# Kernel tuning notes

Hardware: AMD Instinct MI355X
Metric: run time of the kernel (lower is better)

Reference implementation:

```python
import jax, jax.numpy as jnp
import numpy as np
import math

HASHMAP_SIZE = 1 << 17
N_LEVELS = 16
N_FEATURES = 2
BASE_RES = 16.0
GROWTH = 1.5  # per-level resolution growth factor
PRIME_Y = np.uint32(2654435761)  # Instant-NGP spatial hash prime


def hash_encode(x, encoding):
    """Multiresolution 2D hash-grid encoding with bilinear interpolation.
    x: [N, 2] in [0,1); encoding: [T, L, F]. Returns [N, L*F]."""
    N = x.shape[0]
    scales = jnp.asarray(BASE_RES * GROWTH ** np.arange(N_LEVELS),
                         dtype=x.dtype)  # [L]
    pos = x[:, None, :] * scales[None, :, None]        # [N, L, 2]
    pf = jnp.floor(pos)
    frac = pos - pf                                    # [N, L, 2]
    pi = pf.astype(jnp.uint32)                         # integer corner base
    lvl = jnp.arange(N_LEVELS)[None, :]                # [1, L]

    feat = jnp.zeros((N, N_LEVELS, N_FEATURES), dtype=x.dtype)
    for cx in (0, 1):
        for cy in (0, 1):
            ix = pi[..., 0] + jnp.uint32(cx)
            iy = pi[..., 1] + jnp.uint32(cy)
            h = ix ^ (iy * PRIME_Y)                    # spatial hash (wraps mod 2^32)
            idx = (h & jnp.uint32(HASHMAP_SIZE - 1)).astype(jnp.int32)  # [N, L]
            wx = frac[..., 0] if cx else 1.0 - frac[..., 0]
            wy = frac[..., 1] if cy else 1.0 - frac[..., 1]
            feat = feat + (wx * wy)[..., None] * encoding[idx, lvl]  # gather [N,L,F]
    return feat.reshape(N, N_LEVELS * N_FEATURES)


def setup_inputs() -> dict:
    key = jax.random.key(0)
    ks = jax.random.split(key, 8)
    N = 1 << 20
    n_neurons = [32, 64, 64, 3]
    x = jax.random.uniform(ks[0], (N, 2), dtype=jnp.float32)
    # encoding init: rand * 2e-4 - 1e-4
    encoding = jax.random.uniform(ks[1], (HASHMAP_SIZE, N_LEVELS, N_FEATURES),
                                  dtype=jnp.float32) * 2e-4 - 1e-4
    inp = {"x": x, "encoding": encoding}
    for i in range(3):
        s = 1.0 / math.sqrt(n_neurons[i])
        w = jax.random.uniform(ks[2 + i], (n_neurons[i], n_neurons[i + 1]),
                               dtype=jnp.float32) * 2 * s - s
        b = jax.random.uniform(ks[5 + i], (n_neurons[i + 1],),
                               dtype=jnp.float32) * 2 * s - s
        inp[f"w{i}"] = w
        inp[f"b{i}"] = b
    return inp


def reference(x, encoding, w0, b0, w1, b1, w2, b2):
    feat = hash_encode(x, encoding)                 # [N, 32]
    h = jax.nn.relu(feat @ w0 + b0)                 # [N, 64]
    h = jax.nn.relu(h @ w1 + b1)                    # [N, 64]
    return h @ w2 + b2                              # [N, 3]
```

## Files before the change

### kernel.cpp

```cpp
#include <hip/hip_runtime.h>
#include <stdint.h>

typedef __bf16 bf16_t;
typedef bf16_t bf16x8 __attribute__((ext_vector_type(8)));
typedef float  f32x4  __attribute__((ext_vector_type(4)));
typedef float  f32x2v __attribute__((ext_vector_type(2)));

static constexpr uint32_t PRIME = 2654435761u;
static constexpr uint32_t HMASK = (1u << 17) - 1u;
static constexpr uint32_t TSIZE = 1u << 17;

static constexpr int NLDS   = 5308;
static constexpr int NDALL  = 136642;

static constexpr float FSCALE = 8192.0f;
static constexpr float WSCALE = 1.0f / 8192.0f;

__device__ __forceinline__ uint32_t fbits(float f) {
    union { float f; uint32_t u; } v; v.f = f; return v.u;
}
__device__ __forceinline__ float asfloat(uint32_t u) {
    union { uint32_t u; float f; } v; v.u = u; return v.f;
}

__device__ __forceinline__ uint32_t enc8(float v) {
    const uint32_t s = (fbits(v) >> 24) & 0x80u;
    float m = fabsf(v) * 0x1p-120f;
    uint32_t u = fbits(m);
    u += 0x7FFFFu + ((u >> 20) & 1u);
    return s | ((u >> 20) & 0x7fu);
}
__device__ __forceinline__ uint32_t pack8(float a, float b) {
#if __has_builtin(__builtin_amdgcn_cvt_pk_fp8_f32)
    return (uint32_t)__builtin_amdgcn_cvt_pk_fp8_f32(a, b, 0, false) & 0xffffu;
#else
    return enc8(a) | (enc8(b) << 8);
#endif
}
__device__ __forceinline__ float2 unpack8(uint32_t u) {
#if __has_builtin(__builtin_amdgcn_cvt_pk_f32_fp8)
    f32x2v r = __builtin_amdgcn_cvt_pk_f32_fp8((int)u, false);
    return make_float2(r.x, r.y);
#else
    const float f0 = asfloat(((u & 0x80u) << 24) | ((u & 0x7fu) << 20)) * 0x1p120f;
    const float f1 = asfloat(((u & 0x8000u) << 16) | ((u & 0x7f00u) << 12)) * 0x1p120f;
    return make_float2(f0, f1);
#endif
}

__global__ __launch_bounds__(256)
void repack_enc8(const float2* __restrict__ src, uint16_t* __restrict__ dst) {
    __shared__ uint16_t ldsT[8 * 257];
    const int tid = threadIdx.x;
    const int t0  = blockIdx.x * 256;
#pragma unroll
    for (int k = 0; k < 8; ++k) {
        const int j = k * 256 + tid;
        const int tl = j >> 3, l8 = j & 7;
        const float2 f = src[((size_t)(t0 + tl) << 4) + 8 + l8];
        ldsT[l8 * 257 + tl] = (uint16_t)pack8(f.x * FSCALE, f.y * FSCALE);
    }
    __syncthreads();
#pragma unroll
    for (int k = 0; k < 8; ++k)
        dst[((uint32_t)k << 17) + t0 + tid] = ldsT[k * 257 + tid];
}

__global__ __launch_bounds__(256)
void densify_enc(const float2* __restrict__ src, uint16_t* __restrict__ dst) {
    const int i = blockIdx.x * 256 + threadIdx.x;
    if (i >= NDALL) return;
    int lvl, W, off;
    if      (i <   289) { lvl = 0; W =  17; off = 0;     }
    else if (i <   914) { lvl = 1; W =  25; off = 289;   }
    else if (i <  2283) { lvl = 2; W =  37; off = 914;   }
    else if (i <  5308) { lvl = 3; W =  55; off = 2283;  }
    else if (i < 12032) { lvl = 4; W =  82; off = 5308;  }
    else if (i < 27161) { lvl = 5; W = 123; off = 12032; }
    else if (i < 61017) { lvl = 6; W = 184; off = 27161; }
    else                { lvl = 7; W = 275; off = 61017; }
    const int li = i - off;
    const uint32_t iy = (uint32_t)(li / W), ix = (uint32_t)(li % W);
    const uint32_t h = (ix ^ (iy * PRIME)) & HMASK;
    const float2 f = src[h * 16 + lvl];
    dst[i] = (uint16_t)pack8(f.x * FSCALE, f.y * FSCALE);
}

__global__ __launch_bounds__(256)
void pairify_enc(const uint16_t* __restrict__ d16, uint32_t* __restrict__ dst) {
    const int i = blockIdx.x * 256 + threadIdx.x;
    if (i >= NDALL) return;
    const uint32_t a = d16[i];
    const uint32_t b = (i + 1 < NDALL) ? d16[i + 1] : 0u;
    dst[i] = a | (b << 16);
}

__global__ __launch_bounds__(256, 2)
void fused_hash_mlp(const float* __restrict__ xin,
                    const uint16_t* __restrict__ tab8,
                    const uint32_t* __restrict__ dpair,
                    const float* __restrict__ w0, const float* __restrict__ b0,
                    const float* __restrict__ w1, const float* __restrict__ b1,
                    const float* __restrict__ w2, const float* __restrict__ b2,
                    float* __restrict__ out,
                    int nGroups)
{
    __shared__ uint32_t ldsTab[NLDS];
    __shared__ __align__(16) bf16_t lds[4 * 16 * 80];

    const int tid  = threadIdx.x;
    const int wib  = tid >> 6;
    const int lane = tid & 63;
    const int q    = lane >> 4;
    const int n16  = lane & 15;

    bf16_t* myLds = &lds[wib * (16 * 80)];

    for (int i = tid; i < NLDS; i += 256) ldsTab[i] = dpair[i];

    bf16x8 Bw0[4], Bw1[2][4], Bw2[2];
#pragma unroll
    for (int t = 0; t < 4; ++t)
#pragma unroll
        for (int j = 0; j < 8; ++j)
            Bw0[t][j] = (bf16_t)(w0[(q * 8 + j) * 64 + t * 16 + n16] * WSCALE);
#pragma unroll
    for (int c = 0; c < 2; ++c)
#pragma unroll
        for (int t = 0; t < 4; ++t)
#pragma unroll
            for (int j = 0; j < 8; ++j)
                Bw1[c][t][j] = (bf16_t)w1[(c * 32 + q * 8 + j) * 64 + t * 16 + n16];
#pragma unroll
    for (int c = 0; c < 2; ++c)
#pragma unroll
        for (int j = 0; j < 8; ++j)
            Bw2[c][j] = (n16 < 3) ? (bf16_t)w2[(c * 32 + q * 8 + j) * 3 + n16]
                                  : (bf16_t)0.0f;

    float bv0[4], bv1[4];
#pragma unroll
    for (int t = 0; t < 4; ++t) {
        bv0[t] = b0[t * 16 + n16];
        bv1[t] = b1[t * 16 + n16];
    }
    const float bv2 = (n16 < 3) ? b2[n16] : 0.0f;

    const float sb = 16.0f * ((q == 0) ? 1.0f :
                              (q == 1) ? 5.0625f :
                              (q == 2) ? 25.62890625f :
                                         129.746337890625f);
    const float sc[4] = { sb, sb * 1.5f, sb * 2.25f, sb * 3.375f };

    const uint32_t l8base = ((uint32_t)((q >= 2 ? q - 2 : 0) * 4)) << 17;

    __syncthreads();

    for (int g = blockIdx.x; g < nGroups; g += gridDim.x) {
        const int tile = g * 4 + wib;
        const int p = tile * 16 + n16;
        const float2 xy = ((const float2*)xin)[p];
        const float px = xy.x, py = xy.y;

        bf16x8 af;
#pragma unroll
        for (int lv = 0; lv < 4; ++lv) {
            const float posx = px * sc[lv], posy = py * sc[lv];
            const float fx = floorf(posx), fy = floorf(posy);
            const float frx = posx - fx,  fry = posy - fy;
            const uint32_t ix = (uint32_t)fx, iy = (uint32_t)fy;

            const uint32_t Wl = (lv == 0) ? 17u  : (lv == 1) ? 25u
                              : (lv == 2) ? 37u  : 55u;
            const uint32_t Ol = (lv == 0) ? 0u   : (lv == 1) ? 289u
                              : (lv == 2) ? 914u : 2283u;
            const uint32_t Wg = (lv == 0) ? 82u    : (lv == 1) ? 123u
                              : (lv == 2) ? 184u   : 275u;
            const uint32_t Og = (lv == 0) ? 5308u  : (lv == 1) ? 12032u
                              : (lv == 2) ? 27161u : 61017u;

            uint32_t u00, u10, u01, u11;
            if (q == 0) {
                const uint32_t a  = Ol + iy * Wl + ix;
                const uint32_t p0 = ldsTab[a];
                const uint32_t p1 = ldsTab[a + Wl];
                u00 = p0 & 0xffffu; u10 = p0 >> 16;
                u01 = p1 & 0xffffu; u11 = p1 >> 16;
            } else if (q == 1) {
                const uint32_t a  = Og + iy * Wg + ix;
                const uint32_t p0 = dpair[a];
                const uint32_t p1 = dpair[a + Wg];
                u00 = p0 & 0xffffu; u10 = p0 >> 16;
                u01 = p1 & 0xffffu; u11 = p1 >> 16;
            } else {
                const uint32_t hy0 = iy * PRIME, hy1 = hy0 + PRIME;
                const uint32_t i00 = ( ix       ^ hy0) & HMASK;
                const uint32_t i10 = ((ix + 1u) ^ hy0) & HMASK;
                const uint32_t i01 = ( ix       ^ hy1) & HMASK;
                const uint32_t i11 = ((ix + 1u) ^ hy1) & HMASK;
                const uint32_t base = l8base + ((uint32_t)lv << 17);
                u00 = tab8[base + i00];
                u10 = tab8[base + i10];
                u01 = tab8[base + i01];
                u11 = tab8[base + i11];
            }

            const float2 e00 = unpack8(u00);
            const float2 e10 = unpack8(u10);
            const float2 e01 = unpack8(u01);
            const float2 e11 = unpack8(u11);
            const float wx1 = frx, wx0 = 1.0f - frx, wy1 = fry, wy0 = 1.0f - fry;
            const float w00 = wx0 * wy0, w10 = wx1 * wy0, w01 = wx0 * wy1, w11 = wx1 * wy1;
            const float f0 = w00 * e00.x + w10 * e10.x + w01 * e01.x + w11 * e11.x;
            const float f1 = w00 * e00.y + w10 * e10.y + w01 * e01.y + w11 * e11.y;
            af[2 * lv]     = (bf16_t)f0;
            af[2 * lv + 1] = (bf16_t)f1;
        }

        f32x4 c0[4];
#pragma unroll
        for (int t = 0; t < 4; ++t) {
            f32x4 cc = { bv0[t], bv0[t], bv0[t], bv0[t] };
            c0[t] = __builtin_amdgcn_mfma_f32_16x16x32_bf16(af, Bw0[t], cc, 0, 0, 0);
        }

#pragma unroll
        for (int t = 0; t < 4; ++t)
#pragma unroll
            for (int r = 0; r < 4; ++r)
                myLds[(q * 4 + r) * 80 + t * 16 + n16] = (bf16_t)fmaxf(c0[t][r], 0.0f);

        bf16x8 A1[2];
#pragma unroll
        for (int c = 0; c < 2; ++c)
            A1[c] = *(const bf16x8*)&myLds[n16 * 80 + c * 32 + q * 8];

        f32x4 c1[4];
#pragma unroll
        for (int t = 0; t < 4; ++t) {
            f32x4 cc = { bv1[t], bv1[t], bv1[t], bv1[t] };
            cc    = __builtin_amdgcn_mfma_f32_16x16x32_bf16(A1[0], Bw1[0][t], cc, 0, 0, 0);
            c1[t] = __builtin_amdgcn_mfma_f32_16x16x32_bf16(A1[1], Bw1[1][t], cc, 0, 0, 0);
        }

#pragma unroll
        for (int t = 0; t < 4; ++t)
#pragma unroll
            for (int r = 0; r < 4; ++r)
                myLds[(q * 4 + r) * 80 + t * 16 + n16] = (bf16_t)fmaxf(c1[t][r], 0.0f);

        bf16x8 A2[2];
#pragma unroll
        for (int c = 0; c < 2; ++c)
            A2[c] = *(const bf16x8*)&myLds[n16 * 80 + c * 32 + q * 8];

        f32x4 co = { bv2, bv2, bv2, bv2 };
        co = __builtin_amdgcn_mfma_f32_16x16x32_bf16(A2[0], Bw2[0], co, 0, 0, 0);
        co = __builtin_amdgcn_mfma_f32_16x16x32_bf16(A2[1], Bw2[1], co, 0, 0, 0);

        if (n16 < 3) {
#pragma unroll
            for (int r = 0; r < 4; ++r)
                out[(size_t)(tile * 16 + q * 4 + r) * 3 + n16] = co[r];
        }
    }
}

__global__ __launch_bounds__(256)
void fused_hash_mlp_fp32(const float* __restrict__ xin,
                         const float* __restrict__ enc,
                         const float* __restrict__ w0, const float* __restrict__ b0,
                         const float* __restrict__ w1, const float* __restrict__ b1,
                         const float* __restrict__ w2, const float* __restrict__ b2,
                         float* __restrict__ out,
                         int nGroups)
{
    __shared__ __align__(16) bf16_t lds[4 * 16 * 80];
    const int tid  = threadIdx.x;
    const int wib  = tid >> 6;
    const int lane = tid & 63;
    const int q    = lane >> 4;
    const int n16  = lane & 15;
    bf16_t* myLds = &lds[wib * (16 * 80)];

    bf16x8 Bw0[4], Bw1[2][4], Bw2[2];
#pragma unroll
    for (int t = 0; t < 4; ++t)
#pragma unroll
        for (int j = 0; j < 8; ++j)
            Bw0[t][j] = (bf16_t)w0[(q * 8 + j) * 64 + t * 16 + n16];
#pragma unroll
    for (int c = 0; c < 2; ++c)
#pragma unroll
        for (int t = 0; t < 4; ++t)
#pragma unroll
            for (int j = 0; j < 8; ++j)
                Bw1[c][t][j] = (bf16_t)w1[(c * 32 + q * 8 + j) * 64 + t * 16 + n16];
#pragma unroll
    for (int c = 0; c < 2; ++c)
#pragma unroll
        for (int j = 0; j < 8; ++j)
            Bw2[c][j] = (n16 < 3) ? (bf16_t)w2[(c * 32 + q * 8 + j) * 3 + n16]
                                  : (bf16_t)0.0f;

    float bv0[4], bv1[4];
#pragma unroll
    for (int t = 0; t < 4; ++t) { bv0[t] = b0[t * 16 + n16]; bv1[t] = b1[t * 16 + n16]; }
    const float bv2 = (n16 < 3) ? b2[n16] : 0.0f;

    const float sb = 16.0f * ((q == 0) ? 1.0f : (q == 1) ? 5.0625f :
                              (q == 2) ? 25.62890625f : 129.746337890625f);
    const float sc[4] = { sb, sb * 1.5f, sb * 2.25f, sb * 3.375f };
    const char* encB = (const char*)enc;
    const uint32_t lvBase = (uint32_t)q * 32u;

    for (int g = blockIdx.x; g < nGroups; g += gridDim.x) {
        const int tile = g * 4 + wib;
        const int p = tile * 16 + n16;
        const float2 xy = ((const float2*)xin)[p];
        const float px = xy.x, py = xy.y;

        bf16x8 af;
#pragma unroll
        for (int lv = 0; lv < 4; ++lv) {
            const float posx = px * sc[lv], posy = py * sc[lv];
            const float fx = floorf(posx), fy = floorf(posy);
            const float frx = posx - fx,  fry = posy - fy;
            const uint32_t ix = (uint32_t)fx, iy = (uint32_t)fy;
            const uint32_t hy0 = iy * PRIME, hy1 = hy0 + PRIME;
            const uint32_t i00 = ( ix       ^ hy0) & HMASK;
            const uint32_t i10 = ((ix + 1u) ^ hy0) & HMASK;
            const uint32_t i01 = ( ix       ^ hy1) & HMASK;
            const uint32_t i11 = ((ix + 1u) ^ hy1) & HMASK;
            const uint32_t off = lvBase + (uint32_t)lv * 8u;
            const float2 e00 = *(const float2*)(encB + (i00 * 128u + off));
            const float2 e10 = *(const float2*)(encB + (i10 * 128u + off));
            const float2 e01 = *(const float2*)(encB + (i01 * 128u + off));
            const float2 e11 = *(const float2*)(encB + (i11 * 128u + off));
            const float wx1 = frx, wx0 = 1.0f - frx, wy1 = fry, wy0 = 1.0f - fry;
            const float w00 = wx0 * wy0, w10 = wx1 * wy0, w01 = wx0 * wy1, w11 = wx1 * wy1;
            af[2 * lv]     = (bf16_t)(w00 * e00.x + w10 * e10.x + w01 * e01.x + w11 * e11.x);
            af[2 * lv + 1] = (bf16_t)(w00 * e00.y + w10 * e10.y + w01 * e01.y + w11 * e11.y);
        }

        f32x4 c0[4];
#pragma unroll
        for (int t = 0; t < 4; ++t) {
            f32x4 cc = { bv0[t], bv0[t], bv0[t], bv0[t] };
            c0[t] = __builtin_amdgcn_mfma_f32_16x16x32_bf16(af, Bw0[t], cc, 0, 0, 0);
        }
        __syncthreads();
#pragma unroll
        for (int t = 0; t < 4; ++t)
#pragma unroll
            for (int r = 0; r < 4; ++r)
                myLds[(q * 4 + r) * 80 + t * 16 + n16] = (bf16_t)fmaxf(c0[t][r], 0.0f);
        __syncthreads();
        bf16x8 A1[2];
#pragma unroll
        for (int c = 0; c < 2; ++c)
            A1[c] = *(const bf16x8*)&myLds[n16 * 80 + c * 32 + q * 8];

        f32x4 c1[4];
#pragma unroll
        for (int t = 0; t < 4; ++t) {
            f32x4 cc = { bv1[t], bv1[t], bv1[t], bv1[t] };
            cc    = __builtin_amdgcn_mfma_f32_16x16x32_bf16(A1[0], Bw1[0][t], cc, 0, 0, 0);
            c1[t] = __builtin_amdgcn_mfma_f32_16x16x32_bf16(A1[1], Bw1[1][t], cc, 0, 0, 0);
        }
        __syncthreads();
#pragma unroll
        for (int t = 0; t < 4; ++t)
#pragma unroll
            for (int r = 0; r < 4; ++r)
                myLds[(q * 4 + r) * 80 + t * 16 + n16] = (bf16_t)fmaxf(c1[t][r], 0.0f);
        __syncthreads();
        bf16x8 A2[2];
#pragma unroll
        for (int c = 0; c < 2; ++c)
            A2[c] = *(const bf16x8*)&myLds[n16 * 80 + c * 32 + q * 8];

        f32x4 co = { bv2, bv2, bv2, bv2 };
        co = __builtin_amdgcn_mfma_f32_16x16x32_bf16(A2[0], Bw2[0], co, 0, 0, 0);
        co = __builtin_amdgcn_mfma_f32_16x16x32_bf16(A2[1], Bw2[1], co, 0, 0, 0);
        if (n16 < 3) {
#pragma unroll
            for (int r = 0; r < 4; ++r)
                out[(size_t)(tile * 16 + q * 4 + r) * 3 + n16] = co[r];
        }
    }
}

extern "C" void kernel_launch(void* const* d_in, const int* in_sizes, int n_in,
                              void* d_out, int out_size, void* d_ws, size_t ws_size,
                              hipStream_t stream) {
    const float* x  = (const float*)d_in[0];
    const float* en = (const float*)d_in[1];
    const float* w0 = (const float*)d_in[2];
    const float* b0 = (const float*)d_in[3];
    const float* w1 = (const float*)d_in[4];
    const float* b1 = (const float*)d_in[5];
    const float* w2 = (const float*)d_in[6];
    const float* b2 = (const float*)d_in[7];
    float* out = (float*)d_out;

    const int N = in_sizes[0] / 2;
    const int nTiles = N / 16;
    const int nGroups = nTiles / 4;

    const size_t wsNeeded = (size_t)TSIZE * 8 * 2 + (size_t)NDALL * 4 + (size_t)NDALL * 2;
    if (ws_size >= wsNeeded) {
        uint16_t* tab8  = (uint16_t*)d_ws;
        uint32_t* dpair = (uint32_t*)(tab8 + (size_t)TSIZE * 8);
        uint16_t* d16   = (uint16_t*)(dpair + NDALL);
        repack_enc8<<<TSIZE / 256, 256, 0, stream>>>((const float2*)en, tab8);
        densify_enc<<<(NDALL + 255) / 256, 256, 0, stream>>>((const float2*)en, d16);
        pairify_enc<<<(NDALL + 255) / 256, 256, 0, stream>>>(d16, dpair);
        int blocks = 2048;
        if (blocks > nGroups) blocks = nGroups;
        fused_hash_mlp<<<blocks, 256, 0, stream>>>(x, tab8, dpair,
                                                   w0, b0, w1, b1, w2, b2, out, nGroups);
    } else {
        int blocks = 2048;
        if (blocks > nGroups) blocks = nGroups;
        fused_hash_mlp_fp32<<<blocks, 256, 0, stream>>>(x, en, w0, b0, w1, b1, w2, b2, out, nGroups);
    }
}
```

Baseline: 209.1 us.

## Software-pipeline hash gathers with MLP via double-buffered LDS features, wave-per-level split

Reassigns work so each wave gathers one group of four levels for all 64 points of a block group, writing packed bf16 features into a double-buffered LDS array. The gather for the next group is issued before the MLP of the previous group runs, hiding memory latency behind MFMA work. The LDS copy of the dense low-level table is dropped, so those levels are now read from global memory. The change adds a block-wide barrier per iteration and keeps more gathered values live in registers.

```diff
diff --git a/kernel.cpp b/kernel.cpp
--- a/kernel.cpp
+++ b/kernel.cpp
@@ -10,7 +10,6 @@
 static constexpr uint32_t HMASK = (1u << 17) - 1u;
 static constexpr uint32_t TSIZE = 1u << 17;
 
-static constexpr int NLDS   = 5308;
 static constexpr int NDALL  = 136642;
 
 static constexpr float FSCALE = 8192.0f;
@@ -21,6 +20,9 @@
 }
 __device__ __forceinline__ float asfloat(uint32_t u) {
     union { uint32_t u; float f; } v; v.u = u; return v.f;
+}
+__device__ __forceinline__ uint32_t bf16bits(float f) {
+    union { bf16_t h; uint16_t u; } v; v.h = (bf16_t)f; return (uint32_t)v.u;
 }
 
 __device__ __forceinline__ uint32_t enc8(float v) {
@@ -39,7 +41,7 @@
 }
 __device__ __forceinline__ float2 unpack8(uint32_t u) {
 #if __has_builtin(__builtin_amdgcn_cvt_pk_f32_fp8)
-    f32x2v r = __builtin_amdgcn_cvt_pk_f32_fp8((int)u, false);
+    f32x2v r = __builtin_amdgcn_cvt_pk_f32_fp8((int)(u & 0xffffu), false);
     return make_float2(r.x, r.y);
 #else
     const float f0 = asfloat(((u & 0x80u) << 24) | ((u & 0x7fu) << 20)) * 0x1p120f;
@@ -105,7 +107,7 @@
                     float* __restrict__ out,
                     int nGroups)
 {
-    __shared__ uint32_t ldsTab[NLDS];
+    __shared__ __align__(16) uint32_t feat[2][16 * 65];
     __shared__ __align__(16) bf16_t lds[4 * 16 * 80];
 
     const int tid  = threadIdx.x;
@@ -113,10 +115,10 @@
     const int lane = tid & 63;
     const int q    = lane >> 4;
     const int n16  = lane & 15;
+    const int lq   = wib;
+    const int p    = lane;
 
     bf16_t* myLds = &lds[wib * (16 * 80)];
-
-    for (int i = tid; i < NLDS; i += 256) ldsTab[i] = dpair[i];
 
     bf16x8 Bw0[4], Bw1[2][4], Bw2[2];
 #pragma unroll
@@ -146,30 +148,20 @@
     }
     const float bv2 = (n16 < 3) ? b2[n16] : 0.0f;
 
-    const float sb = 16.0f * ((q == 0) ? 1.0f :
-                              (q == 1) ? 5.0625f :
-                              (q == 2) ? 25.62890625f :
-                                         129.746337890625f);
-    const float sc[4] = { sb, sb * 1.5f, sb * 2.25f, sb * 3.375f };
-
-    const uint32_t l8base = ((uint32_t)((q >= 2 ? q - 2 : 0) * 4)) << 17;
-
-    __syncthreads();
-
-    for (int g = blockIdx.x; g < nGroups; g += gridDim.x) {
-        const int tile = g * 4 + wib;
-        const int p = tile * 16 + n16;
-        const float2 xy = ((const float2*)xin)[p];
-        const float px = xy.x, py = xy.y;
-
-        bf16x8 af;
+    const float sbA = 16.0f * ((lq == 0) ? 1.0f :
+                               (lq == 1) ? 5.0625f :
+                               (lq == 2) ? 25.62890625f :
+                                           129.746337890625f);
+    const float scA[4] = { sbA, sbA * 1.5f, sbA * 2.25f, sbA * 3.375f };
+
+    const uint32_t l8base = ((uint32_t)((lq >= 2 ? lq - 2 : 0) * 4)) << 17;
+
+    auto gatherA = [&](int gg, uint32_t (&u)[4][4], float2& xy) {
+        xy = ((const float2*)xin)[gg * 64 + p];
 #pragma unroll
         for (int lv = 0; lv < 4; ++lv) {
-            const float posx = px * sc[lv], posy = py * sc[lv];
-            const float fx = floorf(posx), fy = floorf(posy);
-            const float frx = posx - fx,  fry = posy - fy;
-            const uint32_t ix = (uint32_t)fx, iy = (uint32_t)fy;
-
+            const uint32_t ix = (uint32_t)floorf(xy.x * scA[lv]);
+            const uint32_t iy = (uint32_t)floorf(xy.y * scA[lv]);
             const uint32_t Wl = (lv == 0) ? 17u  : (lv == 1) ? 25u
                               : (lv == 2) ? 37u  : 55u;
             const uint32_t Ol = (lv == 0) ? 0u   : (lv == 1) ? 289u
@@ -178,44 +170,57 @@
                               : (lv == 2) ? 184u   : 275u;
             const uint32_t Og = (lv == 0) ? 5308u  : (lv == 1) ? 12032u
                               : (lv == 2) ? 27161u : 61017u;
-
-            uint32_t u00, u10, u01, u11;
-            if (q == 0) {
-                const uint32_t a  = Ol + iy * Wl + ix;
-                const uint32_t p0 = ldsTab[a];
-                const uint32_t p1 = ldsTab[a + Wl];
-                u00 = p0 & 0xffffu; u10 = p0 >> 16;
-                u01 = p1 & 0xffffu; u11 = p1 >> 16;
-            } else if (q == 1) {
-                const uint32_t a  = Og + iy * Wg + ix;
-                const uint32_t p0 = dpair[a];
-                const uint32_t p1 = dpair[a + Wg];
-                u00 = p0 & 0xffffu; u10 = p0 >> 16;
-                u01 = p1 & 0xffffu; u11 = p1 >> 16;
+            if (lq == 0) {
+                const uint32_t a = Ol + iy * Wl + ix;
+                u[lv][0] = dpair[a];
+                u[lv][1] = dpair[a + Wl];
+            } else if (lq == 1) {
+                const uint32_t a = Og + iy * Wg + ix;
+                u[lv][0] = dpair[a];
+                u[lv][1] = dpair[a + Wg];
             } else {
                 const uint32_t hy0 = iy * PRIME, hy1 = hy0 + PRIME;
-                const uint32_t i00 = ( ix       ^ hy0) & HMASK;
-                const uint32_t i10 = ((ix + 1u) ^ hy0) & HMASK;
-                const uint32_t i01 = ( ix       ^ hy1) & HMASK;
-                const uint32_t i11 = ((ix + 1u) ^ hy1) & HMASK;
                 const uint32_t base = l8base + ((uint32_t)lv << 17);
-                u00 = tab8[base + i00];
-                u10 = tab8[base + i10];
-                u01 = tab8[base + i01];
-                u11 = tab8[base + i11];
+                u[lv][0] = tab8[base + (( ix       ^ hy0) & HMASK)];
+                u[lv][1] = tab8[base + (((ix + 1u) ^ hy0) & HMASK)];
+                u[lv][2] = tab8[base + (( ix       ^ hy1) & HMASK)];
+                u[lv][3] = tab8[base + (((ix + 1u) ^ hy1) & HMASK)];
             }
-
-            const float2 e00 = unpack8(u00);
-            const float2 e10 = unpack8(u10);
-            const float2 e01 = unpack8(u01);
-            const float2 e11 = unpack8(u11);
+        }
+    };
+
+    auto bilerpWrite = [&](int buf, const float2 xy, const uint32_t (&u)[4][4]) {
+#pragma unroll
+        for (int lv = 0; lv < 4; ++lv) {
+            const float posx = xy.x * scA[lv], posy = xy.y * scA[lv];
+            const float frx = posx - floorf(posx);
+            const float fry = posy - floorf(posy);
+            float2 e00, e10, e01, e11;
+            if (lq <= 1) {
+                e00 = unpack8(u[lv][0] & 0xffffu);
+                e10 = unpack8(u[lv][0] >> 16);
+                e01 = unpack8(u[lv][1] & 0xffffu);
+                e11 = unpack8(u[lv][1] >> 16);
+            } else {
+                e00 = unpack8(u[lv][0]);
+                e10 = unpack8(u[lv][1]);
+                e01 = unpack8(u[lv][2]);
+                e11 = unpack8(u[lv][3]);
+            }
             const float wx1 = frx, wx0 = 1.0f - frx, wy1 = fry, wy0 = 1.0f - fry;
             const float w00 = wx0 * wy0, w10 = wx1 * wy0, w01 = wx0 * wy1, w11 = wx1 * wy1;
             const float f0 = w00 * e00.x + w10 * e10.x + w01 * e01.x + w11 * e11.x;
             const float f1 = w00 * e00.y + w10 * e10.y + w01 * e01.y + w11 * e11.y;
-            af[2 * lv]     = (bf16_t)f0;
-            af[2 * lv + 1] = (bf16_t)f1;
-        }
+            feat[buf][(lq * 4 + lv) * 65 + p] = bf16bits(f0) | (bf16bits(f1) << 16);
+        }
+    };
+
+    auto processB = [&](int gg, int buf) {
+        union { uint32_t u[4]; bf16x8 v; } afu;
+#pragma unroll
+        for (int r = 0; r < 4; ++r)
+            afu.u[r] = feat[buf][(q * 4 + r) * 65 + wib * 16 + n16];
+        const bf16x8 af = afu.v;
 
         f32x4 c0[4];
 #pragma unroll
@@ -223,13 +228,11 @@
             f32x4 cc = { bv0[t], bv0[t], bv0[t], bv0[t] };
             c0[t] = __builtin_amdgcn_mfma_f32_16x16x32_bf16(af, Bw0[t], cc, 0, 0, 0);
         }
-
 #pragma unroll
         for (int t = 0; t < 4; ++t)
 #pragma unroll
             for (int r = 0; r < 4; ++r)
                 myLds[(q * 4 + r) * 80 + t * 16 + n16] = (bf16_t)fmaxf(c0[t][r], 0.0f);
-
         bf16x8 A1[2];
 #pragma unroll
         for (int c = 0; c < 2; ++c)
@@ -242,13 +245,11 @@
             cc    = __builtin_amdgcn_mfma_f32_16x16x32_bf16(A1[0], Bw1[0][t], cc, 0, 0, 0);
             c1[t] = __builtin_amdgcn_mfma_f32_16x16x32_bf16(A1[1], Bw1[1][t], cc, 0, 0, 0);
         }
-
 #pragma unroll
         for (int t = 0; t < 4; ++t)
 #pragma unroll
             for (int r = 0; r < 4; ++r)
                 myLds[(q * 4 + r) * 80 + t * 16 + n16] = (bf16_t)fmaxf(c1[t][r], 0.0f);
-
         bf16x8 A2[2];
 #pragma unroll
         for (int c = 0; c < 2; ++c)
@@ -258,12 +259,37 @@
         co = __builtin_amdgcn_mfma_f32_16x16x32_bf16(A2[0], Bw2[0], co, 0, 0, 0);
         co = __builtin_amdgcn_mfma_f32_16x16x32_bf16(A2[1], Bw2[1], co, 0, 0, 0);
 
+        const int tile = gg * 4 + wib;
         if (n16 < 3) {
 #pragma unroll
             for (int r = 0; r < 4; ++r)
                 out[(size_t)(tile * 16 + q * 4 + r) * 3 + n16] = co[r];
         }
+    };
+
+    const int stride = gridDim.x;
+    int g = blockIdx.x;
+    if (g >= nGroups) return;
+
+    uint32_t u[4][4];
+    float2 xy;
+    gatherA(g, u, xy);
+    bilerpWrite(0, xy, u);
+    __syncthreads();
+
+    int it = 0;
+    int gPrev = g;
+    for (g += stride; g < nGroups; g += stride) {
+        uint32_t u2[4][4];
+        float2 xy2;
+        gatherA(g, u2, xy2);
+        processB(gPrev, it & 1);
+        bilerpWrite((it + 1) & 1, xy2, u2);
+        __syncthreads();
+        gPrev = g;
+        ++it;
     }
+    processB(gPrev, it & 1);
 }
 
 __global__ __launch_bounds__(256)
```

After: 251.1 us. +20.1%, slower.

## Assign level groups per wave and exchange encoded features through shared memory

Applied to the files above, without the earlier changes.

The hash-encoding work is redistributed so that each wave handles one quarter of the levels for all 64 points of a group, rather than each lane quarter doing different levels. This removes intra-wave divergence between the LDS-table, dense and hashed branches. Features are exchanged through a double-buffered LDS array with a block barrier per iteration. The coarse levels now read from global dense pairs instead of a preloaded LDS table, trading away the LDS preload and adding a __syncthreads each group.

```diff
diff --git a/kernel.cpp b/kernel.cpp
--- a/kernel.cpp
+++ b/kernel.cpp
@@ -10,7 +10,6 @@
 static constexpr uint32_t HMASK = (1u << 17) - 1u;
 static constexpr uint32_t TSIZE = 1u << 17;
 
-static constexpr int NLDS   = 5308;
 static constexpr int NDALL  = 136642;
 
 static constexpr float FSCALE = 8192.0f;
@@ -21,6 +20,9 @@
 }
 __device__ __forceinline__ float asfloat(uint32_t u) {
     union { uint32_t u; float f; } v; v.u = u; return v.f;
+}
+__device__ __forceinline__ uint32_t bf16bits(float f) {
+    union { bf16_t h; uint16_t u; } v; v.h = (bf16_t)f; return (uint32_t)v.u;
 }
 
 __device__ __forceinline__ uint32_t enc8(float v) {
@@ -39,7 +41,7 @@
 }
 __device__ __forceinline__ float2 unpack8(uint32_t u) {
 #if __has_builtin(__builtin_amdgcn_cvt_pk_f32_fp8)
-    f32x2v r = __builtin_amdgcn_cvt_pk_f32_fp8((int)u, false);
+    f32x2v r = __builtin_amdgcn_cvt_pk_f32_fp8((int)(u & 0xffffu), false);
     return make_float2(r.x, r.y);
 #else
     const float f0 = asfloat(((u & 0x80u) << 24) | ((u & 0x7fu) << 20)) * 0x1p120f;
@@ -105,7 +107,7 @@
                     float* __restrict__ out,
                     int nGroups)
 {
-    __shared__ uint32_t ldsTab[NLDS];
+    __shared__ __align__(16) uint32_t feat[2][16 * 65];
     __shared__ __align__(16) bf16_t lds[4 * 16 * 80];
 
     const int tid  = threadIdx.x;
@@ -113,10 +115,10 @@
     const int lane = tid & 63;
     const int q    = lane >> 4;
     const int n16  = lane & 15;
+    const int lq   = wib;
+    const int p    = lane;
 
     bf16_t* myLds = &lds[wib * (16 * 80)];
-
-    for (int i = tid; i < NLDS; i += 256) ldsTab[i] = dpair[i];
 
     bf16x8 Bw0[4], Bw1[2][4], Bw2[2];
 #pragma unroll
@@ -146,76 +148,85 @@
     }
     const float bv2 = (n16 < 3) ? b2[n16] : 0.0f;
 
-    const float sb = 16.0f * ((q == 0) ? 1.0f :
-                              (q == 1) ? 5.0625f :
-                              (q == 2) ? 25.62890625f :
-                                         129.746337890625f);
-    const float sc[4] = { sb, sb * 1.5f, sb * 2.25f, sb * 3.375f };
-
-    const uint32_t l8base = ((uint32_t)((q >= 2 ? q - 2 : 0) * 4)) << 17;
-
-    __syncthreads();
-
-    for (int g = blockIdx.x; g < nGroups; g += gridDim.x) {
-        const int tile = g * 4 + wib;
-        const int p = tile * 16 + n16;
-        const float2 xy = ((const float2*)xin)[p];
-        const float px = xy.x, py = xy.y;
-
-        bf16x8 af;
-#pragma unroll
-        for (int lv = 0; lv < 4; ++lv) {
-            const float posx = px * sc[lv], posy = py * sc[lv];
-            const float fx = floorf(posx), fy = floorf(posy);
-            const float frx = posx - fx,  fry = posy - fy;
-            const uint32_t ix = (uint32_t)fx, iy = (uint32_t)fy;
-
-            const uint32_t Wl = (lv == 0) ? 17u  : (lv == 1) ? 25u
-                              : (lv == 2) ? 37u  : 55u;
-            const uint32_t Ol = (lv == 0) ? 0u   : (lv == 1) ? 289u
-                              : (lv == 2) ? 914u : 2283u;
-            const uint32_t Wg = (lv == 0) ? 82u    : (lv == 1) ? 123u
-                              : (lv == 2) ? 184u   : 275u;
-            const uint32_t Og = (lv == 0) ? 5308u  : (lv == 1) ? 12032u
-                              : (lv == 2) ? 27161u : 61017u;
-
-            uint32_t u00, u10, u01, u11;
-            if (q == 0) {
-                const uint32_t a  = Ol + iy * Wl + ix;
-                const uint32_t p0 = ldsTab[a];
-                const uint32_t p1 = ldsTab[a + Wl];
-                u00 = p0 & 0xffffu; u10 = p0 >> 16;
-                u01 = p1 & 0xffffu; u11 = p1 >> 16;
-            } else if (q == 1) {
-                const uint32_t a  = Og + iy * Wg + ix;
+    const float sbA = 16.0f * ((lq == 0) ? 1.0f :
+                               (lq == 1) ? 5.0625f :
+                               (lq == 2) ? 25.62890625f :
+                                           129.746337890625f);
+    const float scA0 = sbA,          scA1 = sbA * 1.5f;
+    const float scA2 = sbA * 2.25f,  scA3 = sbA * 3.375f;
+
+    const uint32_t l8base = ((uint32_t)((lq >= 2 ? lq - 2 : 0) * 4)) << 17;
+
+    const int stride = gridDim.x;
+
+    for (int g = blockIdx.x, it = 0; g < nGroups; g += stride, ++it) {
+        const int buf = it & 1;
+        const float2 xy = ((const float2*)xin)[g * 64 + p];
+
+        if (lq >= 2) {
+#pragma unroll
+            for (int lv = 0; lv < 4; ++lv) {
+                const float s = (lv == 0) ? scA0 : (lv == 1) ? scA1
+                              : (lv == 2) ? scA2 : scA3;
+                const float posx = xy.x * s, posy = xy.y * s;
+                const float fx = floorf(posx), fy = floorf(posy);
+                const uint32_t ix = (uint32_t)fx, iy = (uint32_t)fy;
+                const uint32_t hy0 = iy * PRIME, hy1 = hy0 + PRIME;
+                const uint32_t base = l8base + ((uint32_t)lv << 17);
+                const uint32_t u00 = tab8[base + (( ix       ^ hy0) & HMASK)];
+                const uint32_t u10 = tab8[base + (((ix + 1u) ^ hy0) & HMASK)];
+                const uint32_t u01 = tab8[base + (( ix       ^ hy1) & HMASK)];
+                const uint32_t u11 = tab8[base + (((ix + 1u) ^ hy1) & HMASK)];
+                const float frx = posx - fx, fry = posy - fy;
+                const float2 e00 = unpack8(u00);
+                const float2 e10 = unpack8(u10);
+                const float2 e01 = unpack8(u01);
+                const float2 e11 = unpack8(u11);
+                const float wx1 = frx, wx0 = 1.0f - frx, wy1 = fry, wy0 = 1.0f - fry;
+                const float w00 = wx0 * wy0, w10 = wx1 * wy0;
+                const float w01 = wx0 * wy1, w11 = wx1 * wy1;
+                const float f0 = w00 * e00.x + w10 * e10.x + w01 * e01.x + w11 * e11.x;
+                const float f1 = w00 * e00.y + w10 * e10.y + w01 * e01.y + w11 * e11.y;
+                feat[buf][(lq * 4 + lv) * 65 + p] = bf16bits(f0) | (bf16bits(f1) << 16);
+            }
+        } else {
+#pragma unroll
+            for (int lv = 0; lv < 4; ++lv) {
+                const float s = (lv == 0) ? scA0 : (lv == 1) ? scA1
+                              : (lv == 2) ? scA2 : scA3;
+                const uint32_t W = (lq == 0)
+                    ? ((lv == 0) ? 17u : (lv == 1) ? 25u : (lv == 2) ? 37u : 55u)
+                    : ((lv == 0) ? 82u : (lv == 1) ? 123u : (lv == 2) ? 184u : 275u);
+                const uint32_t O = (lq == 0)
+                    ? ((lv == 0) ? 0u : (lv == 1) ? 289u : (lv == 2) ? 914u : 2283u)
+                    : ((lv == 0) ? 5308u : (lv == 1) ? 12032u : (lv == 2) ? 27161u : 61017u);
+                const float posx = xy.x * s, posy = xy.y * s;
+                const float fx = floorf(posx), fy = floorf(posy);
+                const uint32_t ix = (uint32_t)fx, iy = (uint32_t)fy;
+                const uint32_t a = O + iy * W + ix;
                 const uint32_t p0 = dpair[a];
-                const uint32_t p1 = dpair[a + Wg];
-                u00 = p0 & 0xffffu; u10 = p0 >> 16;
-                u01 = p1 & 0xffffu; u11 = p1 >> 16;
-            } else {
-                const uint32_t hy0 = iy * PRIME, hy1 = hy0 + PRIME;
-                const uint32_t i00 = ( ix       ^ hy0) & HMASK;
-                const uint32_t i10 = ((ix + 1u) ^ hy0) & HMASK;
-                const uint32_t i01 = ( ix       ^ hy1) & HMASK;
-                const uint32_t i11 = ((ix + 1u) ^ hy1) & HMASK;
-                const uint32_t base = l8base + ((uint32_t)lv << 17);
-                u00 = tab8[base + i00];
-                u10 = tab8[base + i10];
-                u01 = tab8[base + i01];
-                u11 = tab8[base + i11];
+                const uint32_t p1 = dpair[a + W];
+                const float frx = posx - fx, fry = posy - fy;
+                const float2 e00 = unpack8(p0 & 0xffffu);
+                const float2 e10 = unpack8(p0 >> 16);
+                const float2 e01 = unpack8(p1 & 0xffffu);
+                const float2 e11 = unpack8(p1 >> 16);
+                const float wx1 = frx, wx0 = 1.0f - frx, wy1 = fry, wy0 = 1.0f - fry;
+                const float w00 = wx0 * wy0, w10 = wx1 * wy0;
+                const float w01 = wx0 * wy1, w11 = wx1 * wy1;
+                const float f0 = w00 * e00.x + w10 * e10.x + w01 * e01.x + w11 * e11.x;
+                const float f1 = w00 * e00.y + w10 * e10.y + w01 * e01.y + w11 * e11.y;
+                feat[buf][(lq * 4 + lv) * 65 + p] = bf16bits(f0) | (bf16bits(f1) << 16);
             }
-
-            const float2 e00 = unpack8(u00);
-            const float2 e10 = unpack8(u10);
-            const float2 e01 = unpack8(u01);
-            const float2 e11 = unpack8(u11);
-            const float wx1 = frx, wx0 = 1.0f - frx, wy1 = fry, wy0 = 1.0f - fry;
-            const float w00 = wx0 * wy0, w10 = wx1 * wy0, w01 = wx0 * wy1, w11 = wx1 * wy1;
-            const float f0 = w00 * e00.x + w10 * e10.x + w01 * e01.x + w11 * e11.x;
-            const float f1 = w00 * e00.y + w10 * e10.y + w01 * e01.y + w11 * e11.y;
-            af[2 * lv]     = (bf16_t)f0;
-            af[2 * lv + 1] = (bf16_t)f1;
-        }
+        }
+
+        __syncthreads();
+
+        union { uint32_t u[4]; bf16x8 v; } afu;
+#pragma unroll
+        for (int r = 0; r < 4; ++r)
+            afu.u[r] = feat[buf][(q * 4 + r) * 65 + wib * 16 + n16];
+        const bf16x8 af = afu.v;
 
         f32x4 c0[4];
 #pragma unroll
@@ -223,13 +234,11 @@
             f32x4 cc = { bv0[t], bv0[t], bv0[t], bv0[t] };
             c0[t] = __builtin_amdgcn_mfma_f32_16x16x32_bf16(af, Bw0[t], cc, 0, 0, 0);
         }
-
 #pragma unroll
         for (int t = 0; t < 4; ++t)
 #pragma unroll
             for (int r = 0; r < 4; ++r)
                 myLds[(q * 4 + r) * 80 + t * 16 + n16] = (bf16_t)fmaxf(c0[t][r], 0.0f);
-
         bf16x8 A1[2];
 #pragma unroll
         for (int c = 0; c < 2; ++c)
@@ -242,13 +251,11 @@
             cc    = __builtin_amdgcn_mfma_f32_16x16x32_bf16(A1[0], Bw1[0][t], cc, 0, 0, 0);
             c1[t] = __builtin_amdgcn_mfma_f32_16x16x32_bf16(A1[1], Bw1[1][t], cc, 0, 0, 0);
         }
-
 #pragma unroll
         for (int t = 0; t < 4; ++t)
 #pragma unroll
             for (int r = 0; r < 4; ++r)
                 myLds[(q * 4 + r) * 80 + t * 16 + n16] = (bf16_t)fmaxf(c1[t][r], 0.0f);
-
         bf16x8 A2[2];
 #pragma unroll
         for (int c = 0; c < 2; ++c)
@@ -258,6 +265,7 @@
         co = __builtin_amdgcn_mfma_f32_16x16x32_bf16(A2[0], Bw2[0], co, 0, 0, 0);
         co = __builtin_amdgcn_mfma_f32_16x16x32_bf16(A2[1], Bw2[1], co, 0, 0, 0);
 
+        const int tile = g * 4 + wib;
         if (n16 < 3) {
 #pragma unroll
             for (int r = 0; r < 4; ++r)
```

Result: no change. 211.7 us (+1.3%).
